# Kernel optimization log

Measured on AMD Instinct MI355X. Metric: run time of the kernel, lower is better.

The kernel has to match this reference:

```python
import jax, jax.numpy as jnp
import numpy as np

STATE_DIM = 64
MEASURE_DIM = 32
N = 1048576  # measurement batch (broadcast column dim of z)


def setup_inputs() -> dict:
    key = jax.random.key(0)
    kz, kf = jax.random.split(key)
    z = jax.random.normal(kz, (MEASURE_DIM, N), dtype=jnp.float32)
    # Parameters initialized as in AKF.__init__ (identity matrices), with a
    # small perturbation on F so the dynamics are non-trivial but S stays
    # well-conditioned for the inverse.
    F = jnp.eye(STATE_DIM, dtype=jnp.float32) + 0.01 * jax.random.normal(kf, (STATE_DIM, STATE_DIM), dtype=jnp.float32)
    H = jnp.eye(MEASURE_DIM, STATE_DIM, dtype=jnp.float32)
    Q = jnp.eye(STATE_DIM, dtype=jnp.float32)
    R = jnp.eye(MEASURE_DIM, dtype=jnp.float32)
    P = jnp.eye(STATE_DIM, dtype=jnp.float32)
    x = jnp.zeros((STATE_DIM, 1), dtype=jnp.float32)
    return {"z": z, "F": F, "H": H, "Q": Q, "R": R, "P": P, "x": x}


def reference(z, F, H, Q, R, P, x):
    # One Kalman filter update step (predict + correct), batched over N
    # measurement columns in z. Returns the updated state estimate, matching
    # the torch module's `return self.x`.
    x_pred = F @ x                      # [s, 1]
    P_pred = F @ P @ F.T + Q            # [s, s]
    y = z - H @ x_pred                  # [m, N] (broadcast of [m,1])
    S = H @ P_pred @ H.T + R            # [m, m]
    K = P_pred @ H.T @ jnp.linalg.inv(S)  # [s, m]
    x_new = x_pred + K @ y              # [s, N]
    return x_new
```

## Files before the change

kernel.cpp:

```cpp
#include <hip/hip_runtime.h>

#define SD 64
#define MD 32

typedef float f32x4 __attribute__((ext_vector_type(4)));
typedef float f32x2 __attribute__((ext_vector_type(2)));

__global__ __launch_bounds__(1024) void akf_prepare(
    const float* __restrict__ F, const float* __restrict__ H,
    const float* __restrict__ Q, const float* __restrict__ R,
    const float* __restrict__ P, const float* __restrict__ x,
    float* __restrict__ Kb)
{
    __shared__ __align__(16) float sF [SD * SD];
    __shared__ __align__(16) float sFt[SD * 68];
    __shared__ __align__(16) float sP [SD * SD];
    __shared__ __align__(16) float sT [SD * 68];
    __shared__ __align__(16) float sPp[SD * 68];
    __shared__ __align__(16) float sH [MD * SD];
    __shared__ __align__(16) float sHt[SD * 36];
    __shared__ __align__(16) float sA [SD * 36];
    __shared__ __align__(16) float sS [MD * 33];
    __shared__ __align__(16) float sSi[MD * 36];
    __shared__ __align__(16) float sK [SD * 36];
    __shared__ float sx[SD], sxp[SD], sHx[MD];

    const int tid = threadIdx.x;

    for (int idx = tid; idx < SD * SD; idx += 1024) {
        float f = F[idx], p = P[idx];
        int i = idx >> 6, j = idx & 63;
        sF[idx] = f;
        sFt[j * 68 + i] = f;
        sP[idx] = p;
    }
    for (int idx = tid; idx < MD * SD; idx += 1024) {
        float h = H[idx];
        int j = idx >> 6, k = idx & 63;
        sH[idx] = h;
        sHt[k * 36 + j] = h;
    }
    if (tid < SD) sx[tid] = x[tid];
    __syncthreads();

    if (tid < SD) {
        float a = 0.f;
        for (int k = 0; k < SD; ++k) a = fmaf(sFt[k * 68 + tid], sx[k], a);
        sxp[tid] = a;
    }

    {
        const int i = tid >> 4, j0 = (tid & 15) * 4;
        f32x4 acc = {0.f, 0.f, 0.f, 0.f};
        for (int k = 0; k < SD; ++k) {
            const float f = sF[i * 64 + k];
            const f32x4 p4 = *(const f32x4*)&sP[k * 64 + j0];
            acc.x = fmaf(f, p4.x, acc.x);
            acc.y = fmaf(f, p4.y, acc.y);
            acc.z = fmaf(f, p4.z, acc.z);
            acc.w = fmaf(f, p4.w, acc.w);
        }
        *(f32x4*)&sT[i * 68 + j0] = acc;
    }
    __syncthreads();

    {
        const int i = tid >> 4, j0 = (tid & 15) * 4;
        f32x4 acc = *(const f32x4*)&Q[i * 64 + j0];
        for (int k = 0; k < SD; ++k) {
            const float t = sT[i * 68 + k];
            const f32x4 f4 = *(const f32x4*)&sFt[k * 68 + j0];
            acc.x = fmaf(t, f4.x, acc.x);
            acc.y = fmaf(t, f4.y, acc.y);
            acc.z = fmaf(t, f4.z, acc.z);
            acc.w = fmaf(t, f4.w, acc.w);
        }
        *(f32x4*)&sPp[i * 68 + j0] = acc;
    }
    __syncthreads();

    if (tid < MD) {
        float a = 0.f;
        for (int k = 0; k < SD; ++k) a = fmaf(sHt[k * 36 + tid], sxp[k], a);
        sHx[tid] = a;
    }
    if (tid < 512) {
        const int i = tid >> 3, j0 = (tid & 7) * 4;
        f32x4 acc = {0.f, 0.f, 0.f, 0.f};
        for (int k = 0; k < SD; ++k) {
            const float p = sPp[i * 68 + k];
            const f32x4 h4 = *(const f32x4*)&sHt[k * 36 + j0];
            acc.x = fmaf(p, h4.x, acc.x);
            acc.y = fmaf(p, h4.y, acc.y);
            acc.z = fmaf(p, h4.z, acc.z);
            acc.w = fmaf(p, h4.w, acc.w);
        }
        *(f32x4*)&sA[i * 36 + j0] = acc;
    }
    __syncthreads();

    {
        const int i = tid >> 5, j = tid & 31;
        float a = R[i * 32 + j];
        for (int k = 0; k < SD; ++k) a = fmaf(sH[i * 64 + k], sA[k * 36 + j], a);
        sS[i * 33 + j] = a;
    }
    __syncthreads();

    if (tid < 64) {
        float col[MD];
#pragma unroll
        for (int i = 0; i < MD; ++i)
            col[i] = (tid < MD) ? sS[i * 33 + tid] : ((i == tid - MD) ? 1.f : 0.f);
#pragma unroll
        for (int kp = 0; kp < MD; ++kp) {
            const float piv = __shfl(col[kp], kp);
            const float r = 1.0f / piv;
            col[kp] *= r;
            const float pr = col[kp];
#pragma unroll
            for (int i = 0; i < MD; ++i) {
                if (i == kp) continue;
                const float f = __shfl(col[i], kp);
                col[i] = fmaf(-f, pr, col[i]);
            }
        }
        if (tid >= MD) {
            const int j = tid - MD;
#pragma unroll
            for (int i = 0; i < MD; ++i) sSi[i * 36 + j] = col[i];
        }
    }
    __syncthreads();

    if (tid < 512) {
        const int i = tid >> 3, j0 = (tid & 7) * 4;
        f32x4 acc = {0.f, 0.f, 0.f, 0.f};
        for (int k = 0; k < MD; ++k) {
            const float a = sA[i * 36 + k];
            const f32x4 s4 = *(const f32x4*)&sSi[k * 36 + j0];
            acc.x = fmaf(a, s4.x, acc.x);
            acc.y = fmaf(a, s4.y, acc.y);
            acc.z = fmaf(a, s4.z, acc.z);
            acc.w = fmaf(a, s4.w, acc.w);
        }
        *(f32x4*)&sK[i * 36 + j0] = acc;
        *(f32x4*)&Kb[i * MD + j0] = acc;
    }
    __syncthreads();

    if (tid < SD) {
        float a = sxp[tid];
        for (int j = 0; j < MD; ++j) a = fmaf(-sK[tid * 36 + j], sHx[j], a);
        Kb[SD * MD + tid] = a;
    }
}

__global__ __launch_bounds__(256) void akf_apply(
    const float* __restrict__ z, const float* __restrict__ Kb,
    float* __restrict__ out, int N)
{
    const int c = blockIdx.x * (256 * 2) + threadIdx.x * 2;
    if (c >= N) return;

    f32x2 zv[MD];
#pragma unroll
    for (int j = 0; j < MD; ++j)
        zv[j] = __builtin_nontemporal_load((const f32x2*)(z + (size_t)j * N + c));

#pragma unroll 8
    for (int i = 0; i < SD; ++i) {
        const float bi = Kb[SD * MD + i];
        f32x2 acc = {bi, bi};
#pragma unroll
        for (int j = 0; j < MD; ++j) {
            const float k = Kb[i * MD + j];
            acc.x = fmaf(k, zv[j].x, acc.x);
            acc.y = fmaf(k, zv[j].y, acc.y);
        }
        __builtin_nontemporal_store(acc, (f32x2*)(out + (size_t)i * N + c));
    }
}

extern "C" void kernel_launch(void* const* d_in, const int* in_sizes, int n_in,
                              void* d_out, int out_size, void* d_ws, size_t ws_size,
                              hipStream_t stream)
{
    const float* z = (const float*)d_in[0];
    const float* F = (const float*)d_in[1];
    const float* H = (const float*)d_in[2];
    const float* Q = (const float*)d_in[3];
    const float* R = (const float*)d_in[4];
    const float* P = (const float*)d_in[5];
    const float* x = (const float*)d_in[6];
    float* out = (float*)d_out;
    float* Kb = (float*)d_ws;

    const int N = in_sizes[0] / MD;

    akf_prepare<<<1, 1024, 0, stream>>>(F, H, Q, R, P, x, Kb);

    const int cols_per_block = 256 * 2;
    const int nblocks = (N + cols_per_block - 1) / cols_per_block;
    akf_apply<<<nblocks, 256, 0, stream>>>(z, Kb, out, N);
}
```

Measured before the change: 409.2 us.

## Fuse Kalman gain computation into apply kernel, recomputing per block

Merges the single-block prepare kernel into the streaming apply kernel, so every 1024-thread block recomputes P_pred, S, its inverse and K in shared memory. The z loads are issued before the last gain stages so the memory fetch overlaps that compute. This removes the second launch and the serial dependency on a one-block kernel. In exchange there is a large amount of redundant small-matrix work per block, heavy shared-memory use (around 100 KB), and 1024-thread blocks that lower occupancy for what is a bandwidth-bound stream.

```diff
diff --git a/kernel.cpp b/kernel.cpp
--- a/kernel.cpp
+++ b/kernel.cpp
@@ -6,11 +6,11 @@
 typedef float f32x4 __attribute__((ext_vector_type(4)));
 typedef float f32x2 __attribute__((ext_vector_type(2)));
 
-__global__ __launch_bounds__(1024) void akf_prepare(
-    const float* __restrict__ F, const float* __restrict__ H,
-    const float* __restrict__ Q, const float* __restrict__ R,
-    const float* __restrict__ P, const float* __restrict__ x,
-    float* __restrict__ Kb)
+__global__ __launch_bounds__(1024) void akf_fused(
+    const float* __restrict__ z, const float* __restrict__ F,
+    const float* __restrict__ H, const float* __restrict__ Q,
+    const float* __restrict__ R, const float* __restrict__ P,
+    const float* __restrict__ x, float* __restrict__ out, int N)
 {
     __shared__ __align__(16) float sF [SD * SD];
     __shared__ __align__(16) float sFt[SD * 68];
@@ -23,9 +23,11 @@
     __shared__ __align__(16) float sS [MD * 33];
     __shared__ __align__(16) float sSi[MD * 36];
     __shared__ __align__(16) float sK [SD * 36];
-    __shared__ float sx[SD], sxp[SD], sHx[MD];
+    __shared__ float sx[SD], sxp[SD], sHx[MD], sb[SD];
 
     const int tid = threadIdx.x;
+    const int c = (blockIdx.x * 1024 + tid) * 2;
+    const bool active = (c < N);
 
     for (int idx = tid; idx < SD * SD; idx += 1024) {
         float f = F[idx], p = P[idx];
@@ -133,6 +135,13 @@
     }
     __syncthreads();
 
+    f32x2 zv[MD];
+    if (active) {
+#pragma unroll
+        for (int j = 0; j < MD; ++j)
+            zv[j] = __builtin_nontemporal_load((const f32x2*)(z + (size_t)j * N + c));
+    }
+
     if (tid < 512) {
         const int i = tid >> 3, j0 = (tid & 7) * 4;
         f32x4 acc = {0.f, 0.f, 0.f, 0.f};
@@ -145,40 +154,35 @@
             acc.w = fmaf(a, s4.w, acc.w);
         }
         *(f32x4*)&sK[i * 36 + j0] = acc;
-        *(f32x4*)&Kb[i * MD + j0] = acc;
     }
     __syncthreads();
 
     if (tid < SD) {
         float a = sxp[tid];
         for (int j = 0; j < MD; ++j) a = fmaf(-sK[tid * 36 + j], sHx[j], a);
-        Kb[SD * MD + tid] = a;
-    }
-}
-
-__global__ __launch_bounds__(256) void akf_apply(
-    const float* __restrict__ z, const float* __restrict__ Kb,
-    float* __restrict__ out, int N)
-{
-    const int c = blockIdx.x * (256 * 2) + threadIdx.x * 2;
-    if (c >= N) return;
-
-    f32x2 zv[MD];
-#pragma unroll
-    for (int j = 0; j < MD; ++j)
-        zv[j] = __builtin_nontemporal_load((const f32x2*)(z + (size_t)j * N + c));
-
-#pragma unroll 8
-    for (int i = 0; i < SD; ++i) {
-        const float bi = Kb[SD * MD + i];
-        f32x2 acc = {bi, bi};
-#pragma unroll
-        for (int j = 0; j < MD; ++j) {
-            const float k = Kb[i * MD + j];
-            acc.x = fmaf(k, zv[j].x, acc.x);
-            acc.y = fmaf(k, zv[j].y, acc.y);
-        }
-        __builtin_nontemporal_store(acc, (f32x2*)(out + (size_t)i * N + c));
+        sb[tid] = a;
+    }
+    __syncthreads();
+
+    if (active) {
+#pragma unroll 4
+        for (int i = 0; i < SD; ++i) {
+            const float bi = sb[i];
+            f32x2 acc = {bi, bi};
+#pragma unroll
+            for (int j4 = 0; j4 < MD; j4 += 4) {
+                const f32x4 k4 = *(const f32x4*)&sK[i * 36 + j4];
+                acc.x = fmaf(k4.x, zv[j4 + 0].x, acc.x);
+                acc.y = fmaf(k4.x, zv[j4 + 0].y, acc.y);
+                acc.x = fmaf(k4.y, zv[j4 + 1].x, acc.x);
+                acc.y = fmaf(k4.y, zv[j4 + 1].y, acc.y);
+                acc.x = fmaf(k4.z, zv[j4 + 2].x, acc.x);
+                acc.y = fmaf(k4.z, zv[j4 + 2].y, acc.y);
+                acc.x = fmaf(k4.w, zv[j4 + 3].x, acc.x);
+                acc.y = fmaf(k4.w, zv[j4 + 3].y, acc.y);
+            }
+            __builtin_nontemporal_store(acc, (f32x2*)(out + (size_t)i * N + c));
+        }
     }
 }
 
@@ -194,13 +198,11 @@
     const float* P = (const float*)d_in[5];
     const float* x = (const float*)d_in[6];
     float* out = (float*)d_out;
-    float* Kb = (float*)d_ws;
+    (void)d_ws; (void)ws_size;
 
     const int N = in_sizes[0] / MD;
 
-    akf_prepare<<<1, 1024, 0, stream>>>(F, H, Q, R, P, x, Kb);
-
-    const int cols_per_block = 256 * 2;
+    const int cols_per_block = 1024 * 2;
     const int nblocks = (N + cols_per_block - 1) / cols_per_block;
-    akf_apply<<<nblocks, 256, 0, stream>>>(z, Kb, out, N);
+    akf_fused<<<nblocks, 1024, 0, stream>>>(z, F, H, Q, R, P, x, out, N);
 }
```

Result: slower. 458.8 us (+12.1%).

## Widen apply kernel to float4 columns with two groups per thread, global Kb

Applied to the files above, without the earlier changes.

The apply kernel now processes four columns per thread with 128-bit loads and stores, and each thread handles two column groups in a loop, cutting the block count by four. The K/bias buffer moves from the workspace into a device-global array. Output stores switch from nontemporal to regular stores. This aims to improve memory transaction width and amortize K loads over more columns. In exchange it raises register pressure (32 float4 z values), which may lower occupancy on this bandwidth-bound kernel.

```diff
diff --git a/kernel.cpp b/kernel.cpp
--- a/kernel.cpp
+++ b/kernel.cpp
@@ -5,12 +5,13 @@
 
 typedef float f32x4 __attribute__((ext_vector_type(4)));
 typedef float f32x2 __attribute__((ext_vector_type(2)));
+
+__device__ float g_Kb[SD * MD + SD];
 
 __global__ __launch_bounds__(1024) void akf_prepare(
     const float* __restrict__ F, const float* __restrict__ H,
     const float* __restrict__ Q, const float* __restrict__ R,
-    const float* __restrict__ P, const float* __restrict__ x,
-    float* __restrict__ Kb)
+    const float* __restrict__ P, const float* __restrict__ x)
 {
     __shared__ __align__(16) float sF [SD * SD];
     __shared__ __align__(16) float sFt[SD * 68];
@@ -145,40 +146,47 @@
             acc.w = fmaf(a, s4.w, acc.w);
         }
         *(f32x4*)&sK[i * 36 + j0] = acc;
-        *(f32x4*)&Kb[i * MD + j0] = acc;
+        *(f32x4*)&g_Kb[i * MD + j0] = acc;
     }
     __syncthreads();
 
     if (tid < SD) {
         float a = sxp[tid];
         for (int j = 0; j < MD; ++j) a = fmaf(-sK[tid * 36 + j], sHx[j], a);
-        Kb[SD * MD + tid] = a;
+        g_Kb[SD * MD + tid] = a;
     }
 }
 
 __global__ __launch_bounds__(256) void akf_apply(
-    const float* __restrict__ z, const float* __restrict__ Kb,
-    float* __restrict__ out, int N)
+    const float* __restrict__ z, float* __restrict__ out, int N)
 {
-    const int c = blockIdx.x * (256 * 2) + threadIdx.x * 2;
-    if (c >= N) return;
-
-    f32x2 zv[MD];
-#pragma unroll
-    for (int j = 0; j < MD; ++j)
-        zv[j] = __builtin_nontemporal_load((const f32x2*)(z + (size_t)j * N + c));
-
-#pragma unroll 8
-    for (int i = 0; i < SD; ++i) {
-        const float bi = Kb[SD * MD + i];
-        f32x2 acc = {bi, bi};
-#pragma unroll
-        for (int j = 0; j < MD; ++j) {
-            const float k = Kb[i * MD + j];
-            acc.x = fmaf(k, zv[j].x, acc.x);
-            acc.y = fmaf(k, zv[j].y, acc.y);
-        }
-        __builtin_nontemporal_store(acc, (f32x2*)(out + (size_t)i * N + c));
+    const float* Kb = g_Kb;
+    const int base = blockIdx.x * (256 * 8) + threadIdx.x * 4;
+
+#pragma unroll 1
+    for (int g = 0; g < 2; ++g) {
+        const int c = base + g * (256 * 4);
+        if (c >= N) continue;
+
+        f32x4 zv[MD];
+#pragma unroll
+        for (int j = 0; j < MD; ++j)
+            zv[j] = __builtin_nontemporal_load((const f32x4*)(z + (size_t)j * N + c));
+
+#pragma unroll 4
+        for (int i = 0; i < SD; ++i) {
+            const float bi = Kb[SD * MD + i];
+            f32x4 acc = {bi, bi, bi, bi};
+#pragma unroll
+            for (int j = 0; j < MD; ++j) {
+                const float k = Kb[i * MD + j];
+                acc.x = fmaf(k, zv[j].x, acc.x);
+                acc.y = fmaf(k, zv[j].y, acc.y);
+                acc.z = fmaf(k, zv[j].z, acc.z);
+                acc.w = fmaf(k, zv[j].w, acc.w);
+            }
+            *(f32x4*)(out + (size_t)i * N + c) = acc;
+        }
     }
 }
 
@@ -194,13 +202,13 @@
     const float* P = (const float*)d_in[5];
     const float* x = (const float*)d_in[6];
     float* out = (float*)d_out;
-    float* Kb = (float*)d_ws;
+    (void)d_ws; (void)ws_size;
 
     const int N = in_sizes[0] / MD;
 
-    akf_prepare<<<1, 1024, 0, stream>>>(F, H, Q, R, P, x, Kb);
-
-    const int cols_per_block = 256 * 2;
+    akf_prepare<<<1, 1024, 0, stream>>>(F, H, Q, R, P, x);
+
+    const int cols_per_block = 256 * 8;
     const int nblocks = (N + cols_per_block - 1) / cols_per_block;
-    akf_apply<<<nblocks, 256, 0, stream>>>(z, Kb, out, N);
+    akf_apply<<<nblocks, 256, 0, stream>>>(z, out, N);
 }
```

Measured after the change: 403.2 us. Within noise of the previous version (-1.5%).
